# Performance work log

Hardware: AMD Instinct MI355X
Metric: run time of the kernel (lower is better)

Reference implementation:

```python
import jax, jax.numpy as jnp
import numpy as np

N = 50000      # nodes
E = 800000     # edges (avg degree 16)
IN = 256       # input feature dim
H = 128        # hidden dim
L = 2          # num layers
R = 8          # NUM_RELS_WITH_MASK
RD = 16        # rel_emb_dim
CONF_W = 0.5   # conf_log_weight
LN_EPS = 1e-5


def setup_inputs() -> dict:
    key = jax.random.key(0)
    ks = jax.random.split(key, 12)
    x = jax.random.normal(ks[0], (N, IN), dtype=jnp.float32)
    edge_index = jax.random.randint(ks[1], (2, E), 0, N, dtype=jnp.int32)
    edge_type = jax.random.randint(ks[2], (E,), 0, R, dtype=jnp.int32)
    edge_attr = jax.random.uniform(ks[3], (E, 1), dtype=jnp.float32)
    # encoder input projection (Linear with bias)
    W_in = jax.random.normal(ks[4], (IN, H), dtype=jnp.float32) / np.sqrt(IN)
    b_in = jnp.zeros((H,), dtype=jnp.float32)
    # per-layer params, stacked on leading L dim
    W_msg = jax.random.normal(ks[5], (L, H, H), dtype=jnp.float32) / np.sqrt(H)
    rel_emb = jax.random.normal(ks[6], (L, R, RD), dtype=jnp.float32)
    W_rel = jax.random.normal(ks[7], (L, RD, H), dtype=jnp.float32) / np.sqrt(RD)
    att_vec = jax.random.normal(ks[8], (L, 3 * H), dtype=jnp.float32) / np.sqrt(3 * H)
    bias = jnp.zeros((L, H), dtype=jnp.float32)
    ln_g = jnp.ones((L, H), dtype=jnp.float32)
    ln_b = jnp.zeros((L, H), dtype=jnp.float32)
    return {"x": x, "edge_index": edge_index, "edge_type": edge_type,
            "edge_attr": edge_attr, "W_in": W_in, "b_in": b_in,
            "W_msg": W_msg, "rel_emb": rel_emb, "W_rel": W_rel,
            "att_vec": att_vec, "bias": bias, "ln_g": ln_g, "ln_b": ln_b}


def _layer_norm(h, g, b):
    mu = jnp.mean(h, axis=-1, keepdims=True)
    var = jnp.mean(jnp.square(h - mu), axis=-1, keepdims=True)
    return (h - mu) * jax.lax.rsqrt(var + LN_EPS) * g + b


def reference(x, edge_index, edge_type, edge_attr,
              W_in, b_in, W_msg, rel_emb, W_rel, att_vec, bias, ln_g, ln_b):
    src, dst = edge_index[0], edge_index[1]
    t = jnp.clip(edge_type, 0, R - 1)
    log_conf = CONF_W * jnp.log(jnp.maximum(edge_attr[:, 0], 1e-6))  # [E]

    h = jax.nn.relu(x @ W_in + b_in)  # [N,H]
    for l in range(L):
        # project on nodes first (same math as projecting gathered rows, E >> N)
        hm = h @ W_msg[l]                 # [N,H]
        h_src = hm[src]                   # [E,H]
        h_dst = hm[dst]                   # [E,H]
        r = rel_emb[l][t] @ W_rel[l]      # [E,H]
        a = att_vec[l]
        a_d, a_s, a_r = a[:H], a[H:2 * H], a[2 * H:]
        e = h_dst @ a_d + h_src @ a_s + r @ a_r          # [E]
        e = jax.nn.leaky_relu(e, negative_slope=0.2) + log_conf
        # segment softmax grouped by dst
        m = jax.ops.segment_max(e, dst, num_segments=N)  # [N]
        ex = jnp.exp(e - m[dst])
        s = jax.ops.segment_sum(ex, dst, num_segments=N)  # [N]
        alpha = ex / s[dst]                               # [E]
        msg = h_src * alpha[:, None]                      # [E,H]
        out = jax.ops.segment_sum(msg, dst, num_segments=N) + bias[l]
        h = _layer_norm(h + jax.nn.relu(out), ln_g[l], ln_b[l])
    return h
```

## Files before the change

kernel.cpp:

```cpp
#include <hip/hip_runtime.h>
#include <hip/hip_bf16.h>

#define N_NODES 50000
#define NE      800000
#define IN_DIM  256
#define H_DIM   128
#define NL      2
#define NR      8
#define RD_DIM  16
#define CONF_W  0.5f
#define LN_EPS  1e-5f

#define SCAN_CHUNK 1024
#define NB_SCAN    ((N_NODES + SCAN_CHUNK - 1) / SCAN_CHUNK)
#define DCAP       128

typedef __attribute__((ext_vector_type(8))) short bf16x8;
typedef __attribute__((ext_vector_type(4))) float f32x4;

__device__ __forceinline__ unsigned short f2bf(float f) {
    unsigned u = __float_as_uint(f);
    u += 0x7fffu + ((u >> 16) & 1u);
    return (unsigned short)(u >> 16);
}
__device__ __forceinline__ float bf_lo(unsigned v) {
    return __uint_as_float(v << 16);
}
__device__ __forceinline__ float bf_hi(unsigned v) {
    return __uint_as_float(v & 0xffff0000u);
}


__global__ void k_zero_counts(int* __restrict__ counts) {
    int i = blockIdx.x * 256 + threadIdx.x;
    if (i < N_NODES) counts[i] = 0;
}

__global__ void k_count(const int* __restrict__ dstv, int* __restrict__ counts,
                        int* __restrict__ rank) {
    int i = blockIdx.x * 256 + threadIdx.x;
    if (i >= NE) return;
    rank[i] = atomicAdd(counts + dstv[i], 1);
}

__global__ __launch_bounds__(256) void k_scan1(const int* __restrict__ counts,
                                               int* __restrict__ bsum) {
    __shared__ int lsum[256];
    const int t = threadIdx.x, b = blockIdx.x;
    const int base = b * SCAN_CHUNK + t * 4;
    int s = 0;
#pragma unroll
    for (int j = 0; j < 4; ++j) {
        int idx = base + j;
        if (idx < N_NODES) s += counts[idx];
    }
    lsum[t] = s;
    __syncthreads();
    for (int off = 128; off; off >>= 1) {
        if (t < off) lsum[t] += lsum[t + off];
        __syncthreads();
    }
    if (t == 0) bsum[b] = lsum[0];
}

__global__ void k_scan2(const int* __restrict__ bsum, int* __restrict__ bbase) {
    int lane = threadIdx.x & 63;
    int v = (lane < NB_SCAN) ? bsum[lane] : 0;
    int inc = v;
    for (int off = 1; off < 64; off <<= 1) {
        int tmp = __shfl_up(inc, off);
        if (lane >= off) inc += tmp;
    }
    if (lane < NB_SCAN) bbase[lane] = inc - v;
}

__global__ __launch_bounds__(256) void k_scan3(const int* __restrict__ counts,
                                               const int* __restrict__ bbase,
                                               int* __restrict__ offsets) {
    __shared__ int lsum[256];
    const int t = threadIdx.x, b = blockIdx.x;
    const int base = b * SCAN_CHUNK + t * 4;
    int c[4];
    int s = 0;
#pragma unroll
    for (int j = 0; j < 4; ++j) {
        int idx = base + j;
        c[j] = (idx < N_NODES) ? counts[idx] : 0;
        s += c[j];
    }
    lsum[t] = s;
    __syncthreads();
    for (int off = 1; off < 256; off <<= 1) {
        int v = (t >= off) ? lsum[t - off] : 0;
        __syncthreads();
        lsum[t] += v;
        __syncthreads();
    }
    int run = bbase[b] + lsum[t] - s;
#pragma unroll
    for (int j = 0; j < 4; ++j) {
        int idx = base + j;
        if (idx < N_NODES) { offsets[idx] = run; run += c[j]; }
    }
}

__global__ void k_perm(const int* __restrict__ srcv, const int* __restrict__ dstv,
                       const int* __restrict__ et, const float* __restrict__ ea,
                       const int* __restrict__ offsets, const int* __restrict__ rank,
                       uint2* __restrict__ meta_sorted) {
    int i = blockIdx.x * 256 + threadIdx.x;
    if (i >= NE) return;
    int p = offsets[dstv[i]] + rank[i];
    int t = et[i]; t = t < 0 ? 0 : (t > NR - 1 ? NR - 1 : t);
    float lc = CONF_W * logf(fmaxf(ea[i], 1e-6f));
    meta_sorted[p] = make_uint2((unsigned)srcv[i] | ((unsigned)t << 16),
                                __float_as_uint(lc));
}

__global__ void k_rel_score(const float* __restrict__ rel_emb,
                            const float* __restrict__ W_rel,
                            const float* __restrict__ att_vec,
                            float* __restrict__ rel_score) {
    __shared__ float wvec[NL][RD_DIM];
    int t = threadIdx.x;
    if (t < NL * RD_DIM) {
        int l = t / RD_DIM, d = t % RD_DIM;
        const float* wr = W_rel + ((size_t)l * RD_DIM + d) * H_DIM;
        const float* ar = att_vec + (size_t)l * 3 * H_DIM + 2 * H_DIM;
        float s = 0.f;
        for (int k = 0; k < H_DIM; ++k) s += wr[k] * ar[k];
        wvec[l][d] = s;
    }
    __syncthreads();
    if (t < NL * NR) {
        int l = t / NR, r = t % NR;
        const float* re = rel_emb + ((size_t)l * NR + r) * RD_DIM;
        float s = 0.f;
        for (int d = 0; d < RD_DIM; ++d) s += re[d] * wvec[l][d];
        rel_score[t] = s;
    }
}

__global__ void k_setup(const float* __restrict__ W_in,
                        const float* __restrict__ W_msg,
                        unsigned short* __restrict__ Wt_in,
                        unsigned short* __restrict__ Wt_msg,
                        float* __restrict__ dsc, float* __restrict__ ssc) {
    int i = blockIdx.x * 256 + threadIdx.x;
    if (i < H_DIM * IN_DIM) {
        int n = i >> 8, k = i & 255;
        Wt_in[i] = f2bf(W_in[(size_t)k * H_DIM + n]);
    } else if (i < H_DIM * IN_DIM + NL * H_DIM * H_DIM) {
        int r = i - H_DIM * IN_DIM;
        int l = r >> 14;
        int n = (r >> 7) & 127, k = r & 127;
        Wt_msg[r] = f2bf(W_msg[(size_t)l * H_DIM * H_DIM + (size_t)k * H_DIM + n]);
    }
    if (i < NL * N_NODES) { dsc[i] = 0.f; ssc[i] = 0.f; }
}

template <int K, bool ABF16, bool BIASRELU, bool SCORES>
__global__ __launch_bounds__(256) void k_gemm_mfma(
        const void* __restrict__ Av, const unsigned short* __restrict__ Bt,
        const float* __restrict__ bias,
        unsigned short* __restrict__ Cb, int M,
        const float* __restrict__ att_vec_l,
        float* __restrict__ dsc, float* __restrict__ ssc) {
    __shared__ unsigned short As[128 * 40];
    __shared__ unsigned short Bs[128 * 40];
    const int t = threadIdx.x;
    const int wid = t >> 6, lane = t & 63;
    const int wr = wid >> 1, wc = wid & 1;
    const int lm = lane & 15, lg = lane >> 4;
    const int m0 = blockIdx.x * 128;

    f32x4 acc[4][4] = {};

    for (int k0 = 0; k0 < K; k0 += 32) {
        if (ABF16) {
            const unsigned short* A = (const unsigned short*)Av;
#pragma unroll
            for (int i = 0; i < 2; ++i) {
                int flat = t + i * 256;
                int row = flat >> 2, ch = flat & 3;
                int rm = m0 + row; rm = rm < M ? rm : M - 1;
                uint4 v = *(const uint4*)(A + (size_t)rm * K + k0 + ch * 8);
                *(uint4*)(As + row * 40 + ch * 8) = v;
            }
        } else {
            const float* A = (const float*)Av;
#pragma unroll
            for (int i = 0; i < 4; ++i) {
                int flat = t + i * 256;
                int row = flat >> 3, c4 = flat & 7;
                int rm = m0 + row; rm = rm < M ? rm : M - 1;
                float4 fv = *(const float4*)(A + (size_t)rm * K + k0 + c4 * 4);
                uint2 pk;
                pk.x = (unsigned)f2bf(fv.x) | ((unsigned)f2bf(fv.y) << 16);
                pk.y = (unsigned)f2bf(fv.z) | ((unsigned)f2bf(fv.w) << 16);
                *(uint2*)(As + row * 40 + c4 * 4) = pk;
            }
        }
#pragma unroll
        for (int i = 0; i < 2; ++i) {
            int flat = t + i * 256;
            int row = flat >> 2, ch = flat & 3;
            uint4 v = *(const uint4*)(Bt + (size_t)row * K + k0 + ch * 8);
            *(uint4*)(Bs + row * 40 + ch * 8) = v;
        }
        __syncthreads();
        bf16x8 a[4], b[4];
#pragma unroll
        for (int f = 0; f < 4; ++f) {
            a[f] = *(const bf16x8*)(As + (wr * 64 + f * 16 + lm) * 40 + lg * 8);
            b[f] = *(const bf16x8*)(Bs + (wc * 64 + f * 16 + lm) * 40 + lg * 8);
        }
#pragma unroll
        for (int fm = 0; fm < 4; ++fm)
#pragma unroll
            for (int fn = 0; fn < 4; ++fn)
                acc[fm][fn] = __builtin_amdgcn_mfma_f32_16x16x32_bf16(
                    a[fm], b[fn], acc[fm][fn], 0, 0, 0);
        __syncthreads();
    }

    float av[4], asv[4];
    if (SCORES) {
#pragma unroll
        for (int fn = 0; fn < 4; ++fn) {
            int n = wc * 64 + fn * 16 + lm;
            av[fn]  = att_vec_l[n];
            asv[fn] = att_vec_l[H_DIM + n];
        }
    }

#pragma unroll
    for (int fm = 0; fm < 4; ++fm) {
#pragma unroll
        for (int j = 0; j < 4; ++j) {
            int m = m0 + wr * 64 + fm * 16 + lg * 4 + j;
            bool valid = m < M;
            if (BIASRELU) {
#pragma unroll
                for (int fn = 0; fn < 4; ++fn) {
                    int n = wc * 64 + fn * 16 + lm;
                    float v = fmaxf(acc[fm][fn][j] + bias[n], 0.f);
                    if (valid) Cb[(size_t)m * H_DIM + n] = f2bf(v);
                }
            }
            if (SCORES) {
                float pd = 0.f, ps = 0.f;
#pragma unroll
                for (int fn = 0; fn < 4; ++fn) {
                    int n = wc * 64 + fn * 16 + lm;
                    float v = acc[fm][fn][j];
                    if (valid) Cb[(size_t)m * H_DIM + n] = f2bf(v);
                    pd += v * av[fn];
                    ps += v * asv[fn];
                }
#pragma unroll
                for (int off = 8; off; off >>= 1) {
                    pd += __shfl_xor(pd, off);
                    ps += __shfl_xor(ps, off);
                }
                if (lm == 0 && valid) {
                    atomicAdd(dsc + m, pd);
                    atomicAdd(ssc + m, ps);
                }
            }
        }
    }
}

__global__ __launch_bounds__(256) void k_fused(
        const int* __restrict__ offsets, const int* __restrict__ counts,
        const uint2* __restrict__ meta,
        const float* __restrict__ dsc, const float* __restrict__ ssc,
        const float* __restrict__ rel_l,
        const unsigned short* __restrict__ hm,
        const unsigned short* __restrict__ h_in_bf,
        const float* __restrict__ bias_l, const float* __restrict__ g,
        const float* __restrict__ b,
        float* __restrict__ h_out_f32, unsigned short* __restrict__ h_out_bf) {
    __shared__ float rel_s[NR];
    __shared__ float es[4][DCAP];
    __shared__ unsigned short srcs[4][DCAP];
    if (threadIdx.x < NR) rel_s[threadIdx.x] = rel_l[threadIdx.x];
    __syncthreads();

    const int wave = threadIdx.x >> 6, lane = threadIdx.x & 63;
    const int sub = lane & 15, grp = lane >> 4;
    const int d = blockIdx.x * 4 + wave;

    const int start = offsets[d];
    const int deg = counts[d];
    const float dsc_d = dsc[d];

    float m_l = -1e30f;
    for (int j = lane; j < deg; j += 64) {
        uint2 mv = meta[start + j];
        int s = mv.x & 0xffff;
        float e = dsc_d + ssc[s] + rel_s[(mv.x >> 16) & 7];
        e = (e > 0.f ? e : 0.2f * e) + __uint_as_float(mv.y);
        if (j < DCAP) { es[wave][j] = e; srcs[wave][j] = (unsigned short)s; }
        m_l = fmaxf(m_l, e);
    }
    float m = m_l;
    for (int off = 32; off; off >>= 1) m = fmaxf(m, __shfl_xor(m, off));

    __syncthreads();

    float a0 = 0.f, a1 = 0.f, a2 = 0.f, a3 = 0.f,
          a4 = 0.f, a5 = 0.f, a6 = 0.f, a7 = 0.f;
    float s_part = 0.f;
#pragma unroll 2
    for (int k0 = 0; k0 < deg; k0 += 4) {
        int k = k0 + grp;
        if (k < deg) {
            float e; int s;
            if (k < DCAP) { e = es[wave][k]; s = srcs[wave][k]; }
            else {
                uint2 mv = meta[start + k];
                s = mv.x & 0xffff;
                e = dsc_d + ssc[s] + rel_s[(mv.x >> 16) & 7];
                e = (e > 0.f ? e : 0.2f * e) + __uint_as_float(mv.y);
            }
            float w = __expf(e - m);
            s_part += w;
            uint4 rv = *(const uint4*)(hm + (size_t)s * H_DIM + sub * 8);
            a0 += w * bf_lo(rv.x); a1 += w * bf_hi(rv.x);
            a2 += w * bf_lo(rv.y); a3 += w * bf_hi(rv.y);
            a4 += w * bf_lo(rv.z); a5 += w * bf_hi(rv.z);
            a6 += w * bf_lo(rv.w); a7 += w * bf_hi(rv.w);
        }
    }
    a0 += __shfl_xor(a0, 16); a1 += __shfl_xor(a1, 16);
    a2 += __shfl_xor(a2, 16); a3 += __shfl_xor(a3, 16);
    a4 += __shfl_xor(a4, 16); a5 += __shfl_xor(a5, 16);
    a6 += __shfl_xor(a6, 16); a7 += __shfl_xor(a7, 16);
    s_part += __shfl_xor(s_part, 16);
    a0 += __shfl_xor(a0, 32); a1 += __shfl_xor(a1, 32);
    a2 += __shfl_xor(a2, 32); a3 += __shfl_xor(a3, 32);
    a4 += __shfl_xor(a4, 32); a5 += __shfl_xor(a5, 32);
    a6 += __shfl_xor(a6, 32); a7 += __shfl_xor(a7, 32);
    s_part += __shfl_xor(s_part, 32);

    const float inv = (deg > 0) ? 1.f / s_part : 0.f;

    uint4 hv = *(const uint4*)(h_in_bf + (size_t)d * H_DIM + sub * 8);
    float4 b0 = *(const float4*)(bias_l + sub * 8);
    float4 b1 = *(const float4*)(bias_l + sub * 8 + 4);
    float v0 = bf_lo(hv.x) + fmaxf(a0 * inv + b0.x, 0.f);
    float v1 = bf_hi(hv.x) + fmaxf(a1 * inv + b0.y, 0.f);
    float v2 = bf_lo(hv.y) + fmaxf(a2 * inv + b0.z, 0.f);
    float v3 = bf_hi(hv.y) + fmaxf(a3 * inv + b0.w, 0.f);
    float v4 = bf_lo(hv.z) + fmaxf(a4 * inv + b1.x, 0.f);
    float v5 = bf_hi(hv.z) + fmaxf(a5 * inv + b1.y, 0.f);
    float v6 = bf_lo(hv.w) + fmaxf(a6 * inv + b1.z, 0.f);
    float v7 = bf_hi(hv.w) + fmaxf(a7 * inv + b1.w, 0.f);

    float sum = v0 + v1 + v2 + v3 + v4 + v5 + v6 + v7;
    for (int off = 32; off; off >>= 1) sum += __shfl_xor(sum, off);
    float mu = sum * (1.f / (H_DIM * 4));
    float d0 = v0 - mu, d1 = v1 - mu, d2 = v2 - mu, d3 = v3 - mu;
    float d4 = v4 - mu, d5 = v5 - mu, d6 = v6 - mu, d7 = v7 - mu;
    float vs = d0 * d0 + d1 * d1 + d2 * d2 + d3 * d3 +
               d4 * d4 + d5 * d5 + d6 * d6 + d7 * d7;
    for (int off = 32; off; off >>= 1) vs += __shfl_xor(vs, off);
    float invstd = rsqrtf(vs * (1.f / (H_DIM * 4)) + LN_EPS);

    float4 g0 = *(const float4*)(g + sub * 8);
    float4 g1 = *(const float4*)(g + sub * 8 + 4);
    float4 bb0 = *(const float4*)(b + sub * 8);
    float4 bb1 = *(const float4*)(b + sub * 8 + 4);
    float o0 = d0 * invstd * g0.x + bb0.x;
    float o1 = d1 * invstd * g0.y + bb0.y;
    float o2 = d2 * invstd * g0.z + bb0.z;
    float o3 = d3 * invstd * g0.w + bb0.w;
    float o4 = d4 * invstd * g1.x + bb1.x;
    float o5 = d5 * invstd * g1.y + bb1.y;
    float o6 = d6 * invstd * g1.z + bb1.z;
    float o7 = d7 * invstd * g1.w + bb1.w;

    if (grp == 0) {
        if (h_out_f32) {
            float* p = h_out_f32 + (size_t)d * H_DIM + sub * 8;
            *(float4*)p = make_float4(o0, o1, o2, o3);
            *(float4*)(p + 4) = make_float4(o4, o5, o6, o7);
        }
        if (h_out_bf) {
            uint4 pk;
            pk.x = (unsigned)f2bf(o0) | ((unsigned)f2bf(o1) << 16);
            pk.y = (unsigned)f2bf(o2) | ((unsigned)f2bf(o3) << 16);
            pk.z = (unsigned)f2bf(o4) | ((unsigned)f2bf(o5) << 16);
            pk.w = (unsigned)f2bf(o6) | ((unsigned)f2bf(o7) << 16);
            *(uint4*)(h_out_bf + (size_t)d * H_DIM + sub * 8) = pk;
        }
    }
}

extern "C" void kernel_launch(void* const* d_in, const int* in_sizes, int n_in,
                              void* d_out, int out_size, void* d_ws, size_t ws_size,
                              hipStream_t stream) {
    const float* x         = (const float*)d_in[0];
    const int*   edge_index= (const int*)d_in[1];
    const int*   edge_type = (const int*)d_in[2];
    const float* edge_attr = (const float*)d_in[3];
    const float* W_in      = (const float*)d_in[4];
    const float* b_in      = (const float*)d_in[5];
    const float* W_msg     = (const float*)d_in[6];
    const float* rel_emb   = (const float*)d_in[7];
    const float* W_rel     = (const float*)d_in[8];
    const float* att_vec   = (const float*)d_in[9];
    const float* bias      = (const float*)d_in[10];
    const float* ln_g      = (const float*)d_in[11];
    const float* ln_b      = (const float*)d_in[12];
    float* out = (float*)d_out;

    char* w = (char*)d_ws;
    unsigned short* h_bf = (unsigned short*)w; w += (size_t)N_NODES * H_DIM * 2;
    unsigned short* hm_b = (unsigned short*)w; w += (size_t)N_NODES * H_DIM * 2;
    uint2* meta_sorted = (uint2*)w; w += (size_t)NE * 8;
    int*   rank       = (int*)w;   w += (size_t)NE * 4;
    int*   counts     = (int*)w;   w += (size_t)N_NODES * 4;
    int*   offsets    = (int*)w;   w += (size_t)N_NODES * 4;
    float* dsc        = (float*)w; w += (size_t)NL * N_NODES * 4;
    float* ssc        = (float*)w; w += (size_t)NL * N_NODES * 4;
    unsigned short* Wt_in  = (unsigned short*)w; w += (size_t)H_DIM * IN_DIM * 2;
    unsigned short* Wt_msg = (unsigned short*)w; w += (size_t)NL * H_DIM * H_DIM * 2;
    float* rel_score  = (float*)w; w += 64 * 4;
    int*   bsum       = (int*)w;   w += 64 * 4;
    int*   bbase      = (int*)w;   w += 64 * 4;

    const int* srcv = edge_index;
    const int* dstv = edge_index + NE;

    k_zero_counts<<<(N_NODES + 255) / 256, 256, 0, stream>>>(counts);
    k_count<<<(NE + 255) / 256, 256, 0, stream>>>(dstv, counts, rank);
    k_scan1<<<NB_SCAN, 256, 0, stream>>>(counts, bsum);
    k_scan2<<<1, 64, 0, stream>>>(bsum, bbase);
    k_scan3<<<NB_SCAN, 256, 0, stream>>>(counts, bbase, offsets);
    k_perm<<<(NE + 255) / 256, 256, 0, stream>>>(srcv, dstv, edge_type, edge_attr,
                                                 offsets, rank, meta_sorted);
    k_rel_score<<<1, 256, 0, stream>>>(rel_emb, W_rel, att_vec, rel_score);
    k_setup<<<(NL * N_NODES + 255) / 256, 256, 0, stream>>>(
        W_in, W_msg, Wt_in, Wt_msg, dsc, ssc);

    const int GB = (N_NODES + 127) / 128;
    k_gemm_mfma<IN_DIM, false, true, false><<<GB, 256, 0, stream>>>(
        x, Wt_in, b_in, h_bf, N_NODES, nullptr, nullptr, nullptr);

    for (int l = 0; l < NL; ++l) {
        k_gemm_mfma<H_DIM, true, false, true><<<GB, 256, 0, stream>>>(
            h_bf, Wt_msg + (size_t)l * H_DIM * H_DIM, nullptr, hm_b, N_NODES,
            att_vec + (size_t)l * 3 * H_DIM, dsc + (size_t)l * N_NODES,
            ssc + (size_t)l * N_NODES);
        k_fused<<<N_NODES / 4, 256, 0, stream>>>(
            offsets, counts, meta_sorted,
            dsc + (size_t)l * N_NODES, ssc + (size_t)l * N_NODES,
            rel_score + l * NR, hm_b, h_bf,
            bias + (size_t)l * H_DIM, ln_g + (size_t)l * H_DIM,
            ln_b + (size_t)l * H_DIM,
            (l == NL - 1) ? out : nullptr,
            (l == NL - 1) ? nullptr : h_bf);
    }
}
```

Measured before the change: 309.7 us.

## Precompute softmax weights in LDS, unroll gather by two, fold setup kernels

The aggregation kernel now computes the exp weights and their sum in a separate pass into shared memory, padding the per-wave list to a multiple of 8 with zero weights. The main gather loop then runs branch-free and issues two row loads per iteration using precomputed byte offsets. The zero-counts and relation-score kernels are folded into the setup kernel, cutting two launches, and DCAP is raised to 192 so fewer high-degree nodes take the slow path. The extra pass and larger LDS use may lower occupancy a little.

```diff
diff --git a/kernel.cpp b/kernel.cpp
--- a/kernel.cpp
+++ b/kernel.cpp
@@ -13,7 +13,7 @@
 
 #define SCAN_CHUNK 1024
 #define NB_SCAN    ((N_NODES + SCAN_CHUNK - 1) / SCAN_CHUNK)
-#define DCAP       128
+#define DCAP       192
 
 typedef __attribute__((ext_vector_type(8))) short bf16x8;
 typedef __attribute__((ext_vector_type(4))) float f32x4;
@@ -30,11 +30,6 @@
     return __uint_as_float(v & 0xffff0000u);
 }
 
-
-__global__ void k_zero_counts(int* __restrict__ counts) {
-    int i = blockIdx.x * 256 + threadIdx.x;
-    if (i < N_NODES) counts[i] = 0;
-}
 
 __global__ void k_count(const int* __restrict__ dstv, int* __restrict__ counts,
                         int* __restrict__ rank) {
@@ -117,35 +112,16 @@
                                 __float_as_uint(lc));
 }
 
-__global__ void k_rel_score(const float* __restrict__ rel_emb,
-                            const float* __restrict__ W_rel,
-                            const float* __restrict__ att_vec,
-                            float* __restrict__ rel_score) {
-    __shared__ float wvec[NL][RD_DIM];
-    int t = threadIdx.x;
-    if (t < NL * RD_DIM) {
-        int l = t / RD_DIM, d = t % RD_DIM;
-        const float* wr = W_rel + ((size_t)l * RD_DIM + d) * H_DIM;
-        const float* ar = att_vec + (size_t)l * 3 * H_DIM + 2 * H_DIM;
-        float s = 0.f;
-        for (int k = 0; k < H_DIM; ++k) s += wr[k] * ar[k];
-        wvec[l][d] = s;
-    }
-    __syncthreads();
-    if (t < NL * NR) {
-        int l = t / NR, r = t % NR;
-        const float* re = rel_emb + ((size_t)l * NR + r) * RD_DIM;
-        float s = 0.f;
-        for (int d = 0; d < RD_DIM; ++d) s += re[d] * wvec[l][d];
-        rel_score[t] = s;
-    }
-}
-
 __global__ void k_setup(const float* __restrict__ W_in,
                         const float* __restrict__ W_msg,
+                        const float* __restrict__ rel_emb,
+                        const float* __restrict__ W_rel,
+                        const float* __restrict__ att_vec,
                         unsigned short* __restrict__ Wt_in,
                         unsigned short* __restrict__ Wt_msg,
-                        float* __restrict__ dsc, float* __restrict__ ssc) {
+                        float* __restrict__ dsc, float* __restrict__ ssc,
+                        int* __restrict__ counts,
+                        float* __restrict__ rel_score) {
     int i = blockIdx.x * 256 + threadIdx.x;
     if (i < H_DIM * IN_DIM) {
         int n = i >> 8, k = i & 255;
@@ -157,6 +133,28 @@
         Wt_msg[r] = f2bf(W_msg[(size_t)l * H_DIM * H_DIM + (size_t)k * H_DIM + n]);
     }
     if (i < NL * N_NODES) { dsc[i] = 0.f; ssc[i] = 0.f; }
+    if (i < N_NODES) counts[i] = 0;
+
+    if (blockIdx.x == 0) {
+        __shared__ float wvec[NL][RD_DIM];
+        int t = threadIdx.x;
+        if (t < NL * RD_DIM) {
+            int l = t / RD_DIM, d = t % RD_DIM;
+            const float* wr = W_rel + ((size_t)l * RD_DIM + d) * H_DIM;
+            const float* ar = att_vec + (size_t)l * 3 * H_DIM + 2 * H_DIM;
+            float s = 0.f;
+            for (int k = 0; k < H_DIM; ++k) s += wr[k] * ar[k];
+            wvec[l][d] = s;
+        }
+        __syncthreads();
+        if (t < NL * NR) {
+            int l = t / NR, r = t % NR;
+            const float* re = rel_emb + ((size_t)l * NR + r) * RD_DIM;
+            float s = 0.f;
+            for (int d = 0; d < RD_DIM; ++d) s += re[d] * wvec[l][d];
+            rel_score[t] = s;
+        }
+    }
 }
 
 template <int K, bool ABF16, bool BIASRELU, bool SCORES>
@@ -284,7 +282,7 @@
         float* __restrict__ h_out_f32, unsigned short* __restrict__ h_out_bf) {
     __shared__ float rel_s[NR];
     __shared__ float es[4][DCAP];
-    __shared__ unsigned short srcs[4][DCAP];
+    __shared__ unsigned srcoff[4][DCAP];
     if (threadIdx.x < NR) rel_s[threadIdx.x] = rel_l[threadIdx.x];
     __syncthreads();
 
@@ -295,39 +293,68 @@
     const int start = offsets[d];
     const int deg = counts[d];
     const float dsc_d = dsc[d];
+    const int degc = deg < DCAP ? deg : DCAP;
+    const int degp = (degc + 7) & ~7;
 
     float m_l = -1e30f;
     for (int j = lane; j < deg; j += 64) {
         uint2 mv = meta[start + j];
-        int s = mv.x & 0xffff;
+        unsigned s = mv.x & 0xffff;
         float e = dsc_d + ssc[s] + rel_s[(mv.x >> 16) & 7];
         e = (e > 0.f ? e : 0.2f * e) + __uint_as_float(mv.y);
-        if (j < DCAP) { es[wave][j] = e; srcs[wave][j] = (unsigned short)s; }
+        if (j < DCAP) { es[wave][j] = e; srcoff[wave][j] = s * (H_DIM * 2); }
         m_l = fmaxf(m_l, e);
     }
     float m = m_l;
     for (int off = 32; off; off >>= 1) m = fmaxf(m, __shfl_xor(m, off));
 
+    float s_l = 0.f;
+    for (int j = lane; j < degp; j += 64) {
+        float w = 0.f;
+        if (j < degc) w = __expf(es[wave][j] - m);
+        else srcoff[wave][j] = 0;
+        es[wave][j] = w;
+        s_l += w;
+    }
+    if (deg > DCAP) {
+        for (int j = DCAP + lane; j < deg; j += 64) {
+            uint2 mv = meta[start + j];
+            float e = dsc_d + ssc[mv.x & 0xffff] + rel_s[(mv.x >> 16) & 7];
+            e = (e > 0.f ? e : 0.2f * e) + __uint_as_float(mv.y);
+            s_l += __expf(e - m);
+        }
+    }
+    float ssum = s_l;
+    for (int off = 32; off; off >>= 1) ssum += __shfl_xor(ssum, off);
+
     __syncthreads();
 
     float a0 = 0.f, a1 = 0.f, a2 = 0.f, a3 = 0.f,
           a4 = 0.f, a5 = 0.f, a6 = 0.f, a7 = 0.f;
-    float s_part = 0.f;
-#pragma unroll 2
-    for (int k0 = 0; k0 < deg; k0 += 4) {
-        int k = k0 + grp;
-        if (k < deg) {
-            float e; int s;
-            if (k < DCAP) { e = es[wave][k]; s = srcs[wave][k]; }
-            else {
-                uint2 mv = meta[start + k];
-                s = mv.x & 0xffff;
-                e = dsc_d + ssc[s] + rel_s[(mv.x >> 16) & 7];
-                e = (e > 0.f ? e : 0.2f * e) + __uint_as_float(mv.y);
-            }
+    const char* hmp = (const char*)hm;
+    for (int k0 = 0; k0 < degp; k0 += 8) {
+        int ka = k0 + grp, kb = ka + 4;
+        float wa = es[wave][ka];  unsigned oa = srcoff[wave][ka];
+        float wb = es[wave][kb];  unsigned ob = srcoff[wave][kb];
+        uint4 ra = *(const uint4*)(hmp + oa + sub * 16);
+        uint4 rb = *(const uint4*)(hmp + ob + sub * 16);
+        a0 += wa * bf_lo(ra.x) + wb * bf_lo(rb.x);
+        a1 += wa * bf_hi(ra.x) + wb * bf_hi(rb.x);
+        a2 += wa * bf_lo(ra.y) + wb * bf_lo(rb.y);
+        a3 += wa * bf_hi(ra.y) + wb * bf_hi(rb.y);
+        a4 += wa * bf_lo(ra.z) + wb * bf_lo(rb.z);
+        a5 += wa * bf_hi(ra.z) + wb * bf_hi(rb.z);
+        a6 += wa * bf_lo(ra.w) + wb * bf_lo(rb.w);
+        a7 += wa * bf_hi(ra.w) + wb * bf_hi(rb.w);
+    }
+    if (deg > DCAP) {
+        for (int k = DCAP + grp; k < deg; k += 4) {
+            uint2 mv = meta[start + k];
+            unsigned s = mv.x & 0xffff;
+            float e = dsc_d + ssc[s] + rel_s[(mv.x >> 16) & 7];
+            e = (e > 0.f ? e : 0.2f * e) + __uint_as_float(mv.y);
             float w = __expf(e - m);
-            s_part += w;
-            uint4 rv = *(const uint4*)(hm + (size_t)s * H_DIM + sub * 8);
+            uint4 rv = *(const uint4*)(hmp + s * (H_DIM * 2) + sub * 16);
             a0 += w * bf_lo(rv.x); a1 += w * bf_hi(rv.x);
             a2 += w * bf_lo(rv.y); a3 += w * bf_hi(rv.y);
             a4 += w * bf_lo(rv.z); a5 += w * bf_hi(rv.z);
@@ -338,14 +365,12 @@
     a2 += __shfl_xor(a2, 16); a3 += __shfl_xor(a3, 16);
     a4 += __shfl_xor(a4, 16); a5 += __shfl_xor(a5, 16);
     a6 += __shfl_xor(a6, 16); a7 += __shfl_xor(a7, 16);
-    s_part += __shfl_xor(s_part, 16);
     a0 += __shfl_xor(a0, 32); a1 += __shfl_xor(a1, 32);
     a2 += __shfl_xor(a2, 32); a3 += __shfl_xor(a3, 32);
     a4 += __shfl_xor(a4, 32); a5 += __shfl_xor(a5, 32);
     a6 += __shfl_xor(a6, 32); a7 += __shfl_xor(a7, 32);
-    s_part += __shfl_xor(s_part, 32);
-
-    const float inv = (deg > 0) ? 1.f / s_part : 0.f;
+
+    const float inv = (deg > 0) ? 1.f / ssum : 0.f;
 
     uint4 hv = *(const uint4*)(h_in_bf + (size_t)d * H_DIM + sub * 8);
     float4 b0 = *(const float4*)(bias_l + sub * 8);
@@ -435,16 +460,15 @@
     const int* srcv = edge_index;
     const int* dstv = edge_index + NE;
 
-    k_zero_counts<<<(N_NODES + 255) / 256, 256, 0, stream>>>(counts);
+    k_setup<<<(NL * N_NODES + 255) / 256, 256, 0, stream>>>(
+        W_in, W_msg, rel_emb, W_rel, att_vec, Wt_in, Wt_msg, dsc, ssc, counts,
+        rel_score);
     k_count<<<(NE + 255) / 256, 256, 0, stream>>>(dstv, counts, rank);
     k_scan1<<<NB_SCAN, 256, 0, stream>>>(counts, bsum);
     k_scan2<<<1, 64, 0, stream>>>(bsum, bbase);
     k_scan3<<<NB_SCAN, 256, 0, stream>>>(counts, bbase, offsets);
     k_perm<<<(NE + 255) / 256, 256, 0, stream>>>(srcv, dstv, edge_type, edge_attr,
                                                  offsets, rank, meta_sorted);
-    k_rel_score<<<1, 256, 0, stream>>>(rel_emb, W_rel, att_vec, rel_score);
-    k_setup<<<(NL * N_NODES + 255) / 256, 256, 0, stream>>>(
-        W_in, W_msg, Wt_in, Wt_msg, dsc, ssc);
 
     const int GB = (N_NODES + 127) / 128;
     k_gemm_mfma<IN_DIM, false, true, false><<<GB, 256, 0, stream>>>(
```

Measured after the change: 309.1 us. About the same (-0.2%).
